# Performance work log

Measured on AMD Instinct MI355X. Metric: run time of the kernel, lower is better.

The kernel has to match this reference:

```python
import jax, jax.numpy as jnp
import numpy as np

D_BINS = 59          # cfg.cam_d
BEV_H, BEV_W = 128, 128


def setup_inputs() -> dict:
    key = jax.random.key(0)
    k = jax.random.split(key, 7)
    B, N, Cin, H, W = 4, 6, 256, 16, 44
    C = 80  # cfg.cam_bev_c
    img_feats = jax.random.normal(k[0], (B, N, Cin, H, W), dtype=jnp.float32)
    rots = jax.random.normal(k[1], (B, N, 3, 3), dtype=jnp.float32)
    trans = jax.random.normal(k[2], (B, N, 3), dtype=jnp.float32)
    intrins = jax.random.normal(k[3], (B, N, 3, 3), dtype=jnp.float32)
    # 1x1 conv == per-pixel linear layer: weight (D+C, Cin), bias (D+C,)
    w_depth = jax.random.normal(k[4], (D_BINS + C, Cin), dtype=jnp.float32) / np.sqrt(Cin)
    b_depth = jnp.zeros((D_BINS + C,), dtype=jnp.float32)
    # projected BEV grid indices (what get_geometry produces via randint)
    geom = jax.random.randint(k[5], (B, N, D_BINS, H, W, 2), 0, BEV_H, dtype=jnp.int32)
    return {"img_feats": img_feats, "rots": rots, "trans": trans,
            "intrins": intrins, "w_depth": w_depth, "b_depth": b_depth,
            "geom": geom}


def reference(img_feats, rots, trans, intrins, w_depth, b_depth, geom):
    B, N, Cin, H, W = img_feats.shape
    C = w_depth.shape[0] - D_BINS
    # depth_net: 1x1 conv -> (B, N, D+C, H, W)
    x = jnp.einsum('bnchw,oc->bnohw', img_feats, w_depth) + b_depth[None, None, :, None, None]
    depth = jax.nn.softmax(x[:, :, :D_BINS], axis=2)          # (B,N,D,H,W)
    context = x[:, :, D_BINS:]                                 # (B,N,C,H,W)
    # outer product: (B,N,D,C,H,W) -> (B,N,D,H,W,C)
    frustum = depth[:, :, :, None] * context[:, :, None]
    frustum = jnp.transpose(frustum, (0, 1, 2, 4, 5, 3))
    # voxel pooling: scatter-add frustum points into BEV grid by geom indices
    cell = geom[..., 0] * BEV_W + geom[..., 1]                 # (B,N,D,H,W)
    flat_idx = (jnp.arange(B, dtype=jnp.int32)[:, None] * (BEV_H * BEV_W)
                + cell.reshape(B, -1)).reshape(-1)
    bev = jax.ops.segment_sum(frustum.reshape(-1, C), flat_idx,
                              num_segments=B * BEV_H * BEV_W)
    return bev.reshape(B, BEV_H, BEV_W, C).transpose(0, 3, 1, 2)  # (B,C,bev_h,bev_w)
```

## Files before the change

kernel.cpp:

```cpp
#include <hip/hip_runtime.h>
#include <hip/hip_bf16.h>
#include <math.h>

#define D_BINS 59
#define CTX    80
#define O_TOT  139
#define O_PAD  144
#define K_CIN  256
#define PIXELS 704
#define BNPAIR 24
#define BEVHW  16384
#define NBATCH 4

#define NTILE   128
#define NBUCKET (NBATCH * NTILE)
#define TCELLS  128

#define PXT    32
#define NPXT   22
#define NBLK   (BNPAIR * NPXT)
#define SEGS   (6 * NPXT)
#define EPB    (PXT * D_BINS)

#define CAP    2816
#define CAPP   (CAP + TCELLS * 7)

#define WHL_F      36864
#define CTX_OFF    (WHL_F)
#define CTX_F      (BNPAIR * PIXELS * CTX / 2)
#define CNTMAT_OFF (CTX_OFF + CTX_F)
#define OFSMAT_OFF (CNTMAT_OFF + NBLK * NTILE)
#define PLIST_OFF  (OFSMAT_OFF + NBLK * NTILE)

typedef __attribute__((ext_vector_type(8))) short bf16x8;
typedef __attribute__((ext_vector_type(4))) float f32x4;

__device__ __forceinline__ unsigned short f2bf(float v) {
    __hip_bfloat16 h = __float2bfloat16(v);
    return *reinterpret_cast<unsigned short*>(&h);
}
__device__ __forceinline__ float bf2f(unsigned short u) {
    return __uint_as_float(((unsigned)u) << 16);
}

__global__ __launch_bounds__(256) void wsplit_kernel(
    const float* __restrict__ w, unsigned short* __restrict__ whl)
{
    const int row = blockIdx.x;
    const int col = threadIdx.x;
    const float v = (row < O_TOT) ? w[(size_t)row * K_CIN + col] : 0.f;
    const unsigned short hi = f2bf(v);
    const unsigned short lo = f2bf(v - bf2f(hi));
    whl[row * K_CIN + col]            = hi;
    whl[36864 + row * K_CIN + col]    = lo;
}

__global__ __launch_bounds__(128) void gemm_fused(
    const float* __restrict__ img,
    const unsigned short* __restrict__ whl,
    const float* __restrict__ bias,
    const int*   __restrict__ geom,
    __hip_bfloat16* __restrict__ ctx,
    uint2*       __restrict__ plist,
    int*         __restrict__ cntmat,
    int*         __restrict__ ofsmat)
{
    __shared__ __align__(16) unsigned char sW[2][O_PAD * 64];
    __shared__ __align__(16) unsigned char sI[2][PXT * 64];
    __shared__ float sbias[O_PAD];
    __shared__ int lh[NTILE], lofs[NTILE], lcur[NTILE], sscan[NTILE];

    const int tid  = threadIdx.x;
    const int lane = tid & 63;
    const int wv   = tid >> 6;
    const int bn   = blockIdx.y;
    const int p0   = blockIdx.x * PXT;

    sbias[tid] = bias[tid];
    if (tid < 16) sbias[128 + tid] = (128 + tid < O_TOT) ? bias[128 + tid] : 0.f;
    lh[tid] = 0;

    const float* imgbn = img + (size_t)bn * K_CIN * PIXELS;

    f32x4 acc[9];
#pragma unroll
    for (int t = 0; t < 9; ++t) acc[t] = (f32x4){0.f, 0.f, 0.f, 0.f};

    const int k2  = tid >> 3;
    const int px4 = (tid & 7) * 4;

    for (int ks = 0; ks < 8; ++ks) {
        const int k0 = ks * 32;
        __syncthreads();
#pragma unroll
        for (int pl = 0; pl < 2; ++pl) {
            for (int c = tid; c < 576; c += 128) {
                const int row = c >> 2, g = c & 3;
                const int gs  = g ^ ((row >> 1) & 3);
                *(float4*)&sW[pl][row * 64 + gs * 16] =
                    *(const float4*)&whl[pl * 36864 + row * K_CIN + k0 + g * 8];
            }
        }
        {
            const float4 v0 = *(const float4*)&imgbn[(size_t)(k0 + 2 * k2) * PIXELS + p0 + px4];
            const float4 v1 = *(const float4*)&imgbn[(size_t)(k0 + 2 * k2 + 1) * PIXELS + p0 + px4];
            const float a0[4] = {v0.x, v0.y, v0.z, v0.w};
            const float a1[4] = {v1.x, v1.y, v1.z, v1.w};
#pragma unroll
            for (int j = 0; j < 4; ++j) {
                const int px  = px4 + j;
                const int gs  = (k2 >> 2) ^ ((px >> 1) & 3);
                const int off = px * 64 + gs * 16 + 4 * (k2 & 3);
                const unsigned short h0 = f2bf(a0[j]);
                const unsigned short h1 = f2bf(a1[j]);
                const unsigned short l0 = f2bf(a0[j] - bf2f(h0));
                const unsigned short l1 = f2bf(a1[j] - bf2f(h1));
                *(unsigned*)&sI[0][off] = (unsigned)h0 | ((unsigned)h1 << 16);
                *(unsigned*)&sI[1][off] = (unsigned)l0 | ((unsigned)l1 << 16);
            }
        }
        __syncthreads();
        const int m = lane & 15;
        const int g = lane >> 4;
        const int bpx = wv * 16 + m;
        const int bgs = g ^ ((bpx >> 1) & 3);
        const bf16x8 bhi = *(const bf16x8*)&sI[0][bpx * 64 + bgs * 16];
        const bf16x8 blo = *(const bf16x8*)&sI[1][bpx * 64 + bgs * 16];
#pragma unroll
        for (int t = 0; t < 9; ++t) {
            const int row = t * 16 + m;
            const int ags = g ^ ((row >> 1) & 3);
            const bf16x8 ahi = *(const bf16x8*)&sW[0][row * 64 + ags * 16];
            const bf16x8 alo = *(const bf16x8*)&sW[1][row * 64 + ags * 16];
            acc[t] = __builtin_amdgcn_mfma_f32_16x16x32_bf16(ahi, bhi, acc[t], 0, 0, 0);
            acc[t] = __builtin_amdgcn_mfma_f32_16x16x32_bf16(ahi, blo, acc[t], 0, 0, 0);
            acc[t] = __builtin_amdgcn_mfma_f32_16x16x32_bf16(alo, bhi, acc[t], 0, 0, 0);
        }
    }

    const int m   = lane & 15;
    const int q   = lane >> 4;
    const int px_local = wv * 16 + m;
    const int pxg = p0 + px_local;

#pragma unroll
    for (int t = 0; t < 9; ++t)
#pragma unroll
        for (int r = 0; r < 4; ++r) acc[t][r] += sbias[t * 16 + q * 4 + r];

    float gm = -INFINITY;
#pragma unroll
    for (int t = 0; t < 4; ++t)
#pragma unroll
        for (int r = 0; r < 4; ++r)
            if (16 * t + 4 * q + r < D_BINS) gm = fmaxf(gm, acc[t][r]);
    gm = fmaxf(gm, __shfl_xor(gm, 16));
    gm = fmaxf(gm, __shfl_xor(gm, 32));
    float ls = 0.f;
#pragma unroll
    for (int t = 0; t < 4; ++t)
#pragma unroll
        for (int r = 0; r < 4; ++r)
            if (16 * t + 4 * q + r < D_BINS) {
                const float e = __expf(acc[t][r] - gm);
                acc[t][r] = e;
                ls += e;
            }
    ls += __shfl_xor(ls, 16);
    ls += __shfl_xor(ls, 32);
    const float inv = 1.f / ls;

    __syncthreads();

    unsigned short* sctx = (unsigned short*)&sW[0][0];
    const int2* g2 = (const int2*)geom;
    unsigned bc[4][4];
#pragma unroll
    for (int t = 0; t < 4; ++t)
#pragma unroll
        for (int r = 0; r < 4; ++r) {
            const int o = 16 * t + 4 * q + r;
            if (o < D_BINS) {
                const int2 gg = g2[((size_t)(bn * D_BINS + o)) * PIXELS + pxg];
                const int tile = (gg.x >> 3) * 8 + (gg.y >> 4);
                const int cell = (gg.x & 7) * 16 + (gg.y & 15);
                bc[t][r] = (unsigned)((tile << 7) | cell);
                atomicAdd(&lh[tile], 1);
            }
        }
#pragma unroll
    for (int t = 3; t < 9; ++t)
#pragma unroll
        for (int r = 0; r < 4; ++r) {
            const int c = 16 * t + 4 * q + r - D_BINS;
            if (c >= 0 && c < CTX) sctx[px_local * CTX + c] = f2bf(acc[t][r]);
        }
    __syncthreads();

    sscan[tid] = lh[tid];
    __syncthreads();
#pragma unroll
    for (int off = 1; off < NTILE; off <<= 1) {
        const int t = (tid >= off) ? sscan[tid - off] : 0;
        __syncthreads();
        sscan[tid] += t;
        __syncthreads();
    }
    const int blk = bn * NPXT + blockIdx.x;
    {
        const int excl = sscan[tid] - lh[tid];
        lofs[tid] = excl;
        lcur[tid] = 0;
        cntmat[(size_t)blk * NTILE + tid] = lh[tid];
        ofsmat[(size_t)blk * NTILE + tid] = excl;
    }
    __syncthreads();

    uint2* dst = plist + (size_t)blk * EPB;
    const unsigned ctxoff = (unsigned)((bn * PIXELS + pxg) * CTX);
#pragma unroll
    for (int t = 0; t < 4; ++t)
#pragma unroll
        for (int r = 0; r < 4; ++r) {
            const int o = 16 * t + 4 * q + r;
            if (o < D_BINS) {
                const unsigned u = bc[t][r];
                const int tl = (int)(u >> 7);
                const int pos = lofs[tl] + atomicAdd(&lcur[tl], 1);
                dst[pos] = make_uint2(__float_as_uint(acc[t][r] * inv),
                                      (ctxoff << 7) | (u & 127u));
            }
        }
    {
        const char* sb = (const char*)sctx;
        char* gb = (char*)ctx + ((size_t)(bn * PIXELS) + p0) * CTX * 2;
        for (int i = tid; i < PXT * CTX * 2 / 16; i += 128)
            *(float4*)(gb + i * 16) = *(const float4*)(sb + i * 16);
    }
}

__global__ __launch_bounds__(1024) void gather_kernel(
    const uint2* __restrict__ plist,
    const int*   __restrict__ cntmat,
    const int*   __restrict__ ofsmat,
    const unsigned short* __restrict__ ctx,
    float*       __restrict__ out)
{
    __shared__ float sacc[CTX][TCELLS + 1];
    __shared__ uint2 bufB[CAPP];
    __shared__ int sg[256];
    __shared__ int segcnt[SEGS], segofs[SEGS];
    __shared__ int cellcnt[TCELLS], celloff[TCELLS], cellcur[TCELLS], sc[TCELLS];
    uint2* bufA = (uint2*)sacc;

    const int tid    = threadIdx.x;
    const int wv     = tid >> 6;
    const int lane   = tid & 63;
    const int bucket = blockIdx.x;
    const int b      = bucket >> 7;
    const int tile   = bucket & 127;
    const int blk0   = b * SEGS;

    if (tid < 256) {
        const int c = (tid < SEGS) ? cntmat[(size_t)(blk0 + tid) * NTILE + tile] : 0;
        sg[tid] = c;
        if (tid < SEGS) segcnt[tid] = c;
    }
    __syncthreads();
#pragma unroll
    for (int off = 1; off < 256; off <<= 1) {
        const int t = (tid < 256 && tid >= off) ? sg[tid - off] : 0;
        __syncthreads();
        if (tid < 256) sg[tid] += t;
        __syncthreads();
    }
    if (tid < SEGS) segofs[tid] = sg[tid] - segcnt[tid];
    __syncthreads();
    const int total = sg[255];

    {
        const int sub = lane >> 4;
        const int sl  = lane & 15;
        for (int sgi = wv * 4 + sub; sgi < SEGS; sgi += 64) {
            const int n = segcnt[sgi];
            if (!n) continue;
            const int dstb = segofs[sgi];
            const uint2* sp = plist + (size_t)(blk0 + sgi) * EPB
                              + ofsmat[(size_t)(blk0 + sgi) * NTILE + tile];
            for (int i = sl; i < n; i += 16) {
                const int d = dstb + i;
                if (d < CAP) bufA[d] = sp[i];
            }
        }
    }
    const int ncap = (total < CAP) ? total : CAP;
    __syncthreads();

    if (tid < TCELLS) cellcnt[tid] = 0;
    __syncthreads();
    for (int i = tid; i < ncap; i += 1024)
        atomicAdd(&cellcnt[bufA[i].y & 127u], 1);
    __syncthreads();
    if (tid < TCELLS) sc[tid] = (cellcnt[tid] + 7) & ~7;
    __syncthreads();
#pragma unroll
    for (int off = 1; off < TCELLS; off <<= 1) {
        const int t = (tid < TCELLS && tid >= off) ? sc[tid - off] : 0;
        __syncthreads();
        if (tid < TCELLS) sc[tid] += t;
        __syncthreads();
    }
    if (tid < TCELLS) {
        celloff[tid] = sc[tid] - ((cellcnt[tid] + 7) & ~7);
        cellcur[tid] = 0;
    }
    __syncthreads();
    const int padtotal = sc[TCELLS - 1];
    for (int i = tid; i < padtotal; i += 1024) bufB[i] = make_uint2(0u, 0u);
    __syncthreads();
    for (int i = tid; i < ncap; i += 1024) {
        const uint2 e = bufA[i];
        const int c = (int)(e.y & 127u);
        bufB[celloff[c] + atomicAdd(&cellcur[c], 1)] = e;
    }
    __syncthreads();

    for (int c = wv; c < TCELLS; c += 16) {
        const int s0 = celloff[c];
        const int pc = (cellcnt[c] + 7) & ~7;
        float a0 = 0.f, a1 = 0.f;
        for (int i = 0; i < pc; i += 8) {
            uint2 e[8];
#pragma unroll
            for (int r = 0; r < 8; ++r) e[r] = bufB[s0 + i + r];
            if (lane < 40) {
                unsigned u[8];
#pragma unroll
                for (int r = 0; r < 8; ++r)
                    u[r] = *(const unsigned*)(ctx + (e[r].y >> 7) + 2 * lane);
#pragma unroll
                for (int r = 0; r < 8; ++r) {
                    const float d  = __uint_as_float(e[r].x);
                    a0 += d * __uint_as_float(u[r] << 16);
                    a1 += d * __uint_as_float(u[r] & 0xffff0000u);
                }
            }
        }
        if (lane < 40) {
            sacc[2 * lane][c]     = a0;
            sacc[2 * lane + 1][c] = a1;
        }
    }

    if (total > CAP) {
        for (int sgi = 0; sgi < SEGS; ++sgi) {
            const int dstb = segofs[sgi];
            const int n    = segcnt[sgi];
            if (dstb + n <= CAP) continue;
            const uint2* sp = plist + (size_t)(blk0 + sgi) * EPB
                              + ofsmat[(size_t)(blk0 + sgi) * NTILE + tile];
            const int i0 = (CAP > dstb) ? (CAP - dstb) : 0;
            for (int i = i0; i < n; ++i) {
                const uint2 e = sp[i];
                const int c = (int)(e.y & 127u);
                if ((c & 15) == wv && lane < 40) {
                    const unsigned u = *(const unsigned*)(ctx + (e.y >> 7) + 2 * lane);
                    const float dep = __uint_as_float(e.x);
                    sacc[2 * lane][c]     += dep * __uint_as_float(u << 16);
                    sacc[2 * lane + 1][c] += dep * __uint_as_float(u & 0xffff0000u);
                }
            }
        }
    }
    __syncthreads();

    const int tl = bucket & 127;
    const int tr = tl >> 3;
    const int tc = tl & 7;
    const int c0  = tid >> 4;
    const int col = tid & 15;
#pragma unroll
    for (int cc = c0; cc < CTX; cc += 64) {
#pragma unroll
        for (int r = 0; r < 8; ++r) {
            out[((size_t)(b * CTX + cc)) * BEVHW + (tr * 8 + r) * 128 + tc * 16 + col]
                = sacc[cc][r * 16 + col];
        }
    }
}

extern "C" void kernel_launch(void* const* d_in, const int* in_sizes, int n_in,
                              void* d_out, int out_size, void* d_ws, size_t ws_size,
                              hipStream_t stream)
{
    const float* img  = (const float*)d_in[0];
    const float* w    = (const float*)d_in[4];
    const float* bias = (const float*)d_in[5];
    const int*   geom = (const int*)d_in[6];
    float*       out  = (float*)d_out;

    float* ws = (float*)d_ws;
    unsigned short* whl = (unsigned short*)ws;
    __hip_bfloat16* ctx = (__hip_bfloat16*)(ws + CTX_OFF);
    int*   cntmat = (int*)(ws + CNTMAT_OFF);
    int*   ofsmat = (int*)(ws + OFSMAT_OFF);
    uint2* plist  = (uint2*)(ws + PLIST_OFF);

    wsplit_kernel<<<O_PAD, 256, 0, stream>>>(w, whl);

    {
        dim3 grid(NPXT, BNPAIR);
        gemm_fused<<<grid, 128, 0, stream>>>(img, whl, bias, geom, ctx,
                                             plist, cntmat, ofsmat);
    }

    gather_kernel<<<NBUCKET, 1024, 0, stream>>>(plist, cntmat, ofsmat,
                                                (const unsigned short*)ctx, out);
}
```

Measured before the change: 144.5 us.

## Pre-split image to bf16 hi/lo slabs and double-buffer GEMM with 256 threads

```diff
diff --git a/kernel.cpp b/kernel.cpp
--- a/kernel.cpp
+++ b/kernel.cpp
@@ -25,8 +25,14 @@
 #define CAP    2816
 #define CAPP   (CAP + TCELLS * 7)
 
-#define WHL_F      36864
-#define CTX_OFF    (WHL_F)
+#define WSLAB  20480
+#define ISLAB  4096
+
+#define WHL_OFF    0
+#define WHL_F      (8 * WSLAB / 4)
+#define IMGHL_OFF  (WHL_OFF + WHL_F)
+#define IMGHL_F    (NBLK * 8 * ISLAB / 4)
+#define CTX_OFF    (IMGHL_OFF + IMGHL_F)
 #define CTX_F      (BNPAIR * PIXELS * CTX / 2)
 #define CNTMAT_OFF (CTX_OFF + CTX_F)
 #define OFSMAT_OFF (CNTMAT_OFF + NBLK * NTILE)
@@ -43,21 +49,59 @@
     return __uint_as_float(((unsigned)u) << 16);
 }
 
-__global__ __launch_bounds__(256) void wsplit_kernel(
-    const float* __restrict__ w, unsigned short* __restrict__ whl)
+__global__ __launch_bounds__(256) void prep_kernel(
+    const float* __restrict__ img,
+    const float* __restrict__ w,
+    unsigned short* __restrict__ whl2,
+    unsigned short* __restrict__ imghl)
 {
-    const int row = blockIdx.x;
-    const int col = threadIdx.x;
-    const float v = (row < O_TOT) ? w[(size_t)row * K_CIN + col] : 0.f;
-    const unsigned short hi = f2bf(v);
-    const unsigned short lo = f2bf(v - bf2f(hi));
-    whl[row * K_CIN + col]            = hi;
-    whl[36864 + row * K_CIN + col]    = lo;
-}
-
-__global__ __launch_bounds__(128) void gemm_fused(
-    const float* __restrict__ img,
-    const unsigned short* __restrict__ whl,
+    const int tid = threadIdx.x;
+    if (blockIdx.x < O_PAD) {
+        const int row = blockIdx.x;
+        const float v = (row < O_TOT) ? w[(size_t)row * K_CIN + tid] : 0.f;
+        const unsigned short hi = f2bf(v);
+        const unsigned short lo = f2bf(v - bf2f(hi));
+        const int ks = tid >> 5, kk = tid & 31;
+        const int g = kk >> 3, e = kk & 7;
+        const int gs = g ^ ((row >> 1) & 3);
+        const size_t base = (size_t)ks * (WSLAB / 2) + row * 32 + gs * 8 + e;
+        whl2[base]        = hi;
+        whl2[base + 4608] = lo;
+        if (row < 8) {
+            for (int i = tid; i < 1024; i += 256)
+                whl2[(size_t)row * (WSLAB / 2) + 9216 + i] = 0;
+        }
+    } else {
+        __shared__ unsigned short sbuf[ISLAB / 2];
+        const int id = blockIdx.x - O_PAD;
+        const int bn = id / NPXT, pt = id - bn * NPXT;
+        const float* ib = img + (size_t)bn * K_CIN * PIXELS + pt * PXT;
+        for (int ks = 0; ks < 8; ++ks) {
+            const int kk  = tid >> 3;
+            const int px4 = (tid & 7) * 4;
+            const float4 v = *(const float4*)&ib[(size_t)(ks * 32 + kk) * PIXELS + px4];
+            const float a[4] = {v.x, v.y, v.z, v.w};
+            const int g = kk >> 3, e = kk & 7;
+#pragma unroll
+            for (int j = 0; j < 4; ++j) {
+                const int px = px4 + j;
+                const int gs = g ^ ((px >> 1) & 3);
+                const unsigned short hi = f2bf(a[j]);
+                const unsigned short lo = f2bf(a[j] - bf2f(hi));
+                sbuf[px * 32 + gs * 8 + e]        = hi;
+                sbuf[1024 + px * 32 + gs * 8 + e] = lo;
+            }
+            __syncthreads();
+            unsigned short* ob = imghl + ((size_t)id * 8 + ks) * (ISLAB / 2);
+            *(float4*)&ob[tid * 8] = *(const float4*)&sbuf[tid * 8];
+            __syncthreads();
+        }
+    }
+}
+
+__global__ __launch_bounds__(256) void gemm_fused(
+    const unsigned short* __restrict__ whl2,
+    const unsigned short* __restrict__ imghl,
     const float* __restrict__ bias,
     const int*   __restrict__ geom,
     __hip_bfloat16* __restrict__ ctx,
@@ -65,176 +109,208 @@
     int*         __restrict__ cntmat,
     int*         __restrict__ ofsmat)
 {
-    __shared__ __align__(16) unsigned char sW[2][O_PAD * 64];
-    __shared__ __align__(16) unsigned char sI[2][PXT * 64];
+    __shared__ __align__(16) unsigned char sS[2][WSLAB + ISLAB];
     __shared__ float sbias[O_PAD];
     __shared__ int lh[NTILE], lofs[NTILE], lcur[NTILE], sscan[NTILE];
 
     const int tid  = threadIdx.x;
     const int lane = tid & 63;
     const int wv   = tid >> 6;
+    const int s    = wv & 1;
+    const int h    = wv >> 1;
     const int bn   = blockIdx.y;
-    const int p0   = blockIdx.x * PXT;
-
-    sbias[tid] = bias[tid];
-    if (tid < 16) sbias[128 + tid] = (128 + tid < O_TOT) ? bias[128 + tid] : 0.f;
-    lh[tid] = 0;
-
-    const float* imgbn = img + (size_t)bn * K_CIN * PIXELS;
-
-    f32x4 acc[9];
-#pragma unroll
-    for (int t = 0; t < 9; ++t) acc[t] = (f32x4){0.f, 0.f, 0.f, 0.f};
-
-    const int k2  = tid >> 3;
-    const int px4 = (tid & 7) * 4;
+    const int pt   = blockIdx.x;
+    const int p0   = pt * PXT;
+    const int blkid = bn * NPXT + pt;
+
+    const unsigned char* wsrc = (const unsigned char*)whl2;
+    const unsigned char* isrc = (const unsigned char*)(imghl + (size_t)blkid * 8 * (ISLAB / 2));
+
+    float4 r[6];
+#pragma unroll
+    for (int j = 0; j < 5; ++j)
+        r[j] = *(const float4*)(wsrc + (size_t)tid * 16 + j * 4096);
+    r[5] = *(const float4*)(isrc + (size_t)tid * 16);
+
+    const int m = lane & 15;
+    const int q = lane >> 4;
+    const int pxl = s * 16 + m;
+    const int pxg = p0 + pxl;
+
+    unsigned bc[4][4];
+    if (h == 0) {
+        const int2* g2 = (const int2*)geom;
+#pragma unroll
+        for (int t = 0; t < 4; ++t)
+#pragma unroll
+            for (int r2 = 0; r2 < 4; ++r2) {
+                const int o = 16 * t + 4 * q + r2;
+                if (o < D_BINS) {
+                    const int2 gg = g2[((size_t)(bn * D_BINS + o)) * PIXELS + pxg];
+                    const int tile = (gg.x >> 3) * 8 + (gg.y >> 4);
+                    const int cell = (gg.x & 7) * 16 + (gg.y & 15);
+                    bc[t][r2] = (unsigned)((tile << 7) | cell);
+                }
+            }
+    }
+    if (tid < O_PAD) sbias[tid] = (tid < O_TOT) ? bias[tid] : 0.f;
+    if (tid < NTILE) lh[tid] = 0;
+    __syncthreads();
+
+    if (h == 0) {
+#pragma unroll
+        for (int t = 0; t < 4; ++t)
+#pragma unroll
+            for (int r2 = 0; r2 < 4; ++r2)
+                if (16 * t + 4 * q + r2 < D_BINS) atomicAdd(&lh[bc[t][r2] >> 7], 1);
+    }
+
+#pragma unroll
+    for (int j = 0; j < 5; ++j) *(float4*)&sS[0][tid * 16 + j * 4096] = r[j];
+    *(float4*)&sS[0][WSLAB + tid * 16] = r[5];
+#pragma unroll
+    for (int j = 0; j < 5; ++j)
+        r[j] = *(const float4*)(wsrc + WSLAB + (size_t)tid * 16 + j * 4096);
+    r[5] = *(const float4*)(isrc + ISLAB + (size_t)tid * 16);
+    asm volatile("s_waitcnt lgkmcnt(0)" ::: "memory");
+    __builtin_amdgcn_s_barrier();
+    __builtin_amdgcn_sched_barrier(0);
+
+    f32x4 acc[5];
+#pragma unroll
+    for (int t = 0; t < 5; ++t) acc[t] = (f32x4){0.f, 0.f, 0.f, 0.f};
+
+    const int g   = lane >> 4;
+    const int bpx = pxl;
+    const int bgs = g ^ ((bpx >> 1) & 3);
+    const int nt  = 5 - h;
 
     for (int ks = 0; ks < 8; ++ks) {
-        const int k0 = ks * 32;
-        __syncthreads();
-#pragma unroll
-        for (int pl = 0; pl < 2; ++pl) {
-            for (int c = tid; c < 576; c += 128) {
-                const int row = c >> 2, g = c & 3;
-                const int gs  = g ^ ((row >> 1) & 3);
-                *(float4*)&sW[pl][row * 64 + gs * 16] =
-                    *(const float4*)&whl[pl * 36864 + row * K_CIN + k0 + g * 8];
-            }
-        }
-        {
-            const float4 v0 = *(const float4*)&imgbn[(size_t)(k0 + 2 * k2) * PIXELS + p0 + px4];
-            const float4 v1 = *(const float4*)&imgbn[(size_t)(k0 + 2 * k2 + 1) * PIXELS + p0 + px4];
-            const float a0[4] = {v0.x, v0.y, v0.z, v0.w};
-            const float a1[4] = {v1.x, v1.y, v1.z, v1.w};
-#pragma unroll
-            for (int j = 0; j < 4; ++j) {
-                const int px  = px4 + j;
-                const int gs  = (k2 >> 2) ^ ((px >> 1) & 3);
-                const int off = px * 64 + gs * 16 + 4 * (k2 & 3);
-                const unsigned short h0 = f2bf(a0[j]);
-                const unsigned short h1 = f2bf(a1[j]);
-                const unsigned short l0 = f2bf(a0[j] - bf2f(h0));
-                const unsigned short l1 = f2bf(a1[j] - bf2f(h1));
-                *(unsigned*)&sI[0][off] = (unsigned)h0 | ((unsigned)h1 << 16);
-                *(unsigned*)&sI[1][off] = (unsigned)l0 | ((unsigned)l1 << 16);
-            }
-        }
-        __syncthreads();
-        const int m = lane & 15;
-        const int g = lane >> 4;
-        const int bpx = wv * 16 + m;
-        const int bgs = g ^ ((bpx >> 1) & 3);
-        const bf16x8 bhi = *(const bf16x8*)&sI[0][bpx * 64 + bgs * 16];
-        const bf16x8 blo = *(const bf16x8*)&sI[1][bpx * 64 + bgs * 16];
-#pragma unroll
-        for (int t = 0; t < 9; ++t) {
-            const int row = t * 16 + m;
-            const int ags = g ^ ((row >> 1) & 3);
-            const bf16x8 ahi = *(const bf16x8*)&sW[0][row * 64 + ags * 16];
-            const bf16x8 alo = *(const bf16x8*)&sW[1][row * 64 + ags * 16];
-            acc[t] = __builtin_amdgcn_mfma_f32_16x16x32_bf16(ahi, bhi, acc[t], 0, 0, 0);
-            acc[t] = __builtin_amdgcn_mfma_f32_16x16x32_bf16(ahi, blo, acc[t], 0, 0, 0);
-            acc[t] = __builtin_amdgcn_mfma_f32_16x16x32_bf16(alo, bhi, acc[t], 0, 0, 0);
-        }
-    }
-
-    const int m   = lane & 15;
-    const int q   = lane >> 4;
-    const int px_local = wv * 16 + m;
-    const int pxg = p0 + px_local;
-
-#pragma unroll
-    for (int t = 0; t < 9; ++t)
-#pragma unroll
-        for (int r = 0; r < 4; ++r) acc[t][r] += sbias[t * 16 + q * 4 + r];
-
-    float gm = -INFINITY;
-#pragma unroll
-    for (int t = 0; t < 4; ++t)
-#pragma unroll
-        for (int r = 0; r < 4; ++r)
-            if (16 * t + 4 * q + r < D_BINS) gm = fmaxf(gm, acc[t][r]);
-    gm = fmaxf(gm, __shfl_xor(gm, 16));
-    gm = fmaxf(gm, __shfl_xor(gm, 32));
-    float ls = 0.f;
-#pragma unroll
-    for (int t = 0; t < 4; ++t)
-#pragma unroll
-        for (int r = 0; r < 4; ++r)
-            if (16 * t + 4 * q + r < D_BINS) {
-                const float e = __expf(acc[t][r] - gm);
-                acc[t][r] = e;
-                ls += e;
-            }
-    ls += __shfl_xor(ls, 16);
-    ls += __shfl_xor(ls, 32);
-    const float inv = 1.f / ls;
-
-    __syncthreads();
-
-    unsigned short* sctx = (unsigned short*)&sW[0][0];
-    const int2* g2 = (const int2*)geom;
-    unsigned bc[4][4];
-#pragma unroll
-    for (int t = 0; t < 4; ++t)
-#pragma unroll
-        for (int r = 0; r < 4; ++r) {
-            const int o = 16 * t + 4 * q + r;
-            if (o < D_BINS) {
-                const int2 gg = g2[((size_t)(bn * D_BINS + o)) * PIXELS + pxg];
-                const int tile = (gg.x >> 3) * 8 + (gg.y >> 4);
-                const int cell = (gg.x & 7) * 16 + (gg.y & 15);
-                bc[t][r] = (unsigned)((tile << 7) | cell);
-                atomicAdd(&lh[tile], 1);
-            }
-        }
-#pragma unroll
-    for (int t = 3; t < 9; ++t)
-#pragma unroll
-        for (int r = 0; r < 4; ++r) {
-            const int c = 16 * t + 4 * q + r - D_BINS;
-            if (c >= 0 && c < CTX) sctx[px_local * CTX + c] = f2bf(acc[t][r]);
-        }
-    __syncthreads();
-
-    sscan[tid] = lh[tid];
+        const unsigned char* base = sS[ks & 1];
+        const bf16x8 bhi = *(const bf16x8*)&base[WSLAB + bpx * 64 + bgs * 16];
+        const bf16x8 blo = *(const bf16x8*)&base[WSLAB + 2048 + bpx * 64 + bgs * 16];
+#pragma unroll
+        for (int t = 0; t < 5; ++t) {
+            if (t < nt) {
+                const int row = h * 80 + t * 16 + m;
+                const int ags = g ^ ((row >> 1) & 3);
+                const bf16x8 ahi = *(const bf16x8*)&base[row * 64 + ags * 16];
+                const bf16x8 alo = *(const bf16x8*)&base[9216 + row * 64 + ags * 16];
+                acc[t] = __builtin_amdgcn_mfma_f32_16x16x32_bf16(ahi, bhi, acc[t], 0, 0, 0);
+                acc[t] = __builtin_amdgcn_mfma_f32_16x16x32_bf16(ahi, blo, acc[t], 0, 0, 0);
+                acc[t] = __builtin_amdgcn_mfma_f32_16x16x32_bf16(alo, bhi, acc[t], 0, 0, 0);
+            }
+        }
+        if (ks < 7) {
+            __syncthreads();
+            unsigned char* nb = sS[(ks + 1) & 1];
+#pragma unroll
+            for (int j = 0; j < 5; ++j) *(float4*)&nb[tid * 16 + j * 4096] = r[j];
+            *(float4*)&nb[WSLAB + tid * 16] = r[5];
+            if (ks < 6) {
+#pragma unroll
+                for (int j = 0; j < 5; ++j)
+                    r[j] = *(const float4*)(wsrc + (size_t)(ks + 2) * WSLAB + (size_t)tid * 16 + j * 4096);
+                r[5] = *(const float4*)(isrc + (size_t)(ks + 2) * ISLAB + (size_t)tid * 16);
+            }
+            asm volatile("s_waitcnt lgkmcnt(0)" ::: "memory");
+            __builtin_amdgcn_s_barrier();
+            __builtin_amdgcn_sched_barrier(0);
+        }
+    }
+    __syncthreads();
+
+#pragma unroll
+    for (int t = 0; t < 5; ++t)
+        if (t < nt)
+#pragma unroll
+            for (int r2 = 0; r2 < 4; ++r2)
+                acc[t][r2] += sbias[h * 80 + t * 16 + q * 4 + r2];
+
+    float inv = 0.f;
+    if (h == 0) {
+        float gm = -INFINITY;
+#pragma unroll
+        for (int t = 0; t < 4; ++t)
+#pragma unroll
+            for (int r2 = 0; r2 < 4; ++r2)
+                if (16 * t + 4 * q + r2 < D_BINS) gm = fmaxf(gm, acc[t][r2]);
+        gm = fmaxf(gm, __shfl_xor(gm, 16));
+        gm = fmaxf(gm, __shfl_xor(gm, 32));
+        float ls = 0.f;
+#pragma unroll
+        for (int t = 0; t < 4; ++t)
+#pragma unroll
+            for (int r2 = 0; r2 < 4; ++r2)
+                if (16 * t + 4 * q + r2 < D_BINS) {
+                    const float e = __expf(acc[t][r2] - gm);
+                    acc[t][r2] = e;
+                    ls += e;
+                }
+        ls += __shfl_xor(ls, 16);
+        ls += __shfl_xor(ls, 32);
+        inv = 1.f / ls;
+    }
+
+    unsigned short* sctx = (unsigned short*)&sS[0][0];
+    if (h == 0) {
+#pragma unroll
+        for (int t = 3; t < 5; ++t)
+#pragma unroll
+            for (int r2 = 0; r2 < 4; ++r2) {
+                const int c = 16 * t + 4 * q + r2 - D_BINS;
+                if (c >= 0) sctx[pxl * CTX + c] = f2bf(acc[t][r2]);
+            }
+    } else {
+#pragma unroll
+        for (int t = 0; t < 4; ++t)
+#pragma unroll
+            for (int r2 = 0; r2 < 4; ++r2) {
+                const int c = 80 + 16 * t + 4 * q + r2 - D_BINS;
+                if (c < CTX) sctx[pxl * CTX + c] = f2bf(acc[t][r2]);
+            }
+    }
+    __syncthreads();
+
+    if (tid < NTILE) sscan[tid] = lh[tid];
     __syncthreads();
 #pragma unroll
     for (int off = 1; off < NTILE; off <<= 1) {
-        const int t = (tid >= off) ? sscan[tid - off] : 0;
-        __syncthreads();
-        sscan[tid] += t;
-        __syncthreads();
-    }
-    const int blk = bn * NPXT + blockIdx.x;
-    {
+        const int t = (tid < NTILE && tid >= off) ? sscan[tid - off] : 0;
+        __syncthreads();
+        if (tid < NTILE) sscan[tid] += t;
+        __syncthreads();
+    }
+    if (tid < NTILE) {
         const int excl = sscan[tid] - lh[tid];
         lofs[tid] = excl;
         lcur[tid] = 0;
-        cntmat[(size_t)blk * NTILE + tid] = lh[tid];
-        ofsmat[(size_t)blk * NTILE + tid] = excl;
-    }
-    __syncthreads();
-
-    uint2* dst = plist + (size_t)blk * EPB;
-    const unsigned ctxoff = (unsigned)((bn * PIXELS + pxg) * CTX);
-#pragma unroll
-    for (int t = 0; t < 4; ++t)
-#pragma unroll
-        for (int r = 0; r < 4; ++r) {
-            const int o = 16 * t + 4 * q + r;
-            if (o < D_BINS) {
-                const unsigned u = bc[t][r];
-                const int tl = (int)(u >> 7);
-                const int pos = lofs[tl] + atomicAdd(&lcur[tl], 1);
-                dst[pos] = make_uint2(__float_as_uint(acc[t][r] * inv),
-                                      (ctxoff << 7) | (u & 127u));
-            }
-        }
+        cntmat[(size_t)blkid * NTILE + tid] = lh[tid];
+        ofsmat[(size_t)blkid * NTILE + tid] = excl;
+    }
+    __syncthreads();
+
+    if (h == 0) {
+        uint2* dst = plist + (size_t)blkid * EPB;
+        const unsigned ctxoff = (unsigned)((bn * PIXELS + pxg) * CTX);
+#pragma unroll
+        for (int t = 0; t < 4; ++t)
+#pragma unroll
+            for (int r2 = 0; r2 < 4; ++r2) {
+                const int o = 16 * t + 4 * q + r2;
+                if (o < D_BINS) {
+                    const unsigned u = bc[t][r2];
+                    const int tl = (int)(u >> 7);
+                    const int pos = lofs[tl] + atomicAdd(&lcur[tl], 1);
+                    dst[pos] = make_uint2(__float_as_uint(acc[t][r2] * inv),
+                                          (ctxoff << 7) | (u & 127u));
+                }
+            }
+    }
     {
         const char* sb = (const char*)sctx;
         char* gb = (char*)ctx + ((size_t)(bn * PIXELS) + p0) * CTX * 2;
-        for (int i = tid; i < PXT * CTX * 2 / 16; i += 128)
+        for (int i = tid; i < PXT * CTX * 2 / 16; i += 256)
             *(float4*)(gb + i * 16) = *(const float4*)(sb + i * 16);
     }
 }
@@ -400,17 +476,18 @@
     float*       out  = (float*)d_out;
 
     float* ws = (float*)d_ws;
-    unsigned short* whl = (unsigned short*)ws;
+    unsigned short* whl2  = (unsigned short*)(ws + WHL_OFF);
+    unsigned short* imghl = (unsigned short*)(ws + IMGHL_OFF);
     __hip_bfloat16* ctx = (__hip_bfloat16*)(ws + CTX_OFF);
     int*   cntmat = (int*)(ws + CNTMAT_OFF);
     int*   ofsmat = (int*)(ws + OFSMAT_OFF);
     uint2* plist  = (uint2*)(ws + PLIST_OFF);
 
-    wsplit_kernel<<<O_PAD, 256, 0, stream>>>(w, whl);
+    prep_kernel<<<O_PAD + NBLK, 256, 0, stream>>>(img, w, whl2, imghl);
 
     {
         dim3 grid(NPXT, BNPAIR);
-        gemm_fused<<<grid, 128, 0, stream>>>(img, whl, bias, geom, ctx,
+        gemm_fused<<<grid, 256, 0, stream>>>(whl2, imghl, bias, geom, ctx,
                                              plist, cntmat, ofsmat);
     }
 
```

After: 175.5 us. +21.5%, slower.

## Split GEMM into depth and context blocks with single-wave 16-pixel tiles

Applied to the files above, without the earlier changes.

```diff
diff --git a/kernel.cpp b/kernel.cpp
--- a/kernel.cpp
+++ b/kernel.cpp
@@ -5,7 +5,6 @@
 #define D_BINS 59
 #define CTX    80
 #define O_TOT  139
-#define O_PAD  144
 #define K_CIN  256
 #define PIXELS 704
 #define BNPAIR 24
@@ -16,8 +15,8 @@
 #define NBUCKET (NBATCH * NTILE)
 #define TCELLS  128
 
-#define PXT    32
-#define NPXT   22
+#define PXT    16
+#define NPXT   44
 #define NBLK   (BNPAIR * NPXT)
 #define SEGS   (6 * NPXT)
 #define EPB    (PXT * D_BINS)
@@ -25,8 +24,9 @@
 #define CAP    2816
 #define CAPP   (CAP + TCELLS * 7)
 
+#define WHL_OFF    0
 #define WHL_F      36864
-#define CTX_OFF    (WHL_F)
+#define CTX_OFF    (WHL_OFF + WHL_F)
 #define CTX_F      (BNPAIR * PIXELS * CTX / 2)
 #define CNTMAT_OFF (CTX_OFF + CTX_F)
 #define OFSMAT_OFF (CNTMAT_OFF + NBLK * NTILE)
@@ -51,11 +51,41 @@
     const float v = (row < O_TOT) ? w[(size_t)row * K_CIN + col] : 0.f;
     const unsigned short hi = f2bf(v);
     const unsigned short lo = f2bf(v - bf2f(hi));
-    whl[row * K_CIN + col]            = hi;
-    whl[36864 + row * K_CIN + col]    = lo;
-}
-
-__global__ __launch_bounds__(128) void gemm_fused(
+    whl[row * K_CIN + col]         = hi;
+    whl[36864 + row * K_CIN + col] = lo;
+}
+
+template<int NT, int T0>
+__device__ __forceinline__ void kloop(
+    const float* __restrict__ ib, const unsigned short* __restrict__ whl,
+    int pxg, int m, int g, f32x4* acc)
+{
+#pragma unroll 2
+    for (int ks = 0; ks < 8; ++ks) {
+        float bv[8];
+#pragma unroll
+        for (int j = 0; j < 8; ++j)
+            bv[j] = ib[(size_t)(ks * 32 + 8 * g + j) * PIXELS + pxg];
+        bf16x8 bhi, blo;
+#pragma unroll
+        for (int j = 0; j < 8; ++j) {
+            const unsigned short h = f2bf(bv[j]);
+            bhi[j] = (short)h;
+            blo[j] = (short)f2bf(bv[j] - bf2f(h));
+        }
+#pragma unroll
+        for (int t = 0; t < NT; ++t) {
+            const int row = (T0 + t) * 16 + m;
+            const bf16x8 ahi = *(const bf16x8*)&whl[(size_t)row * K_CIN + ks * 32 + g * 8];
+            const bf16x8 alo = *(const bf16x8*)&whl[36864 + (size_t)row * K_CIN + ks * 32 + g * 8];
+            acc[t] = __builtin_amdgcn_mfma_f32_16x16x32_bf16(ahi, bhi, acc[t], 0, 0, 0);
+            acc[t] = __builtin_amdgcn_mfma_f32_16x16x32_bf16(ahi, blo, acc[t], 0, 0, 0);
+            acc[t] = __builtin_amdgcn_mfma_f32_16x16x32_bf16(alo, bhi, acc[t], 0, 0, 0);
+        }
+    }
+}
+
+__global__ __launch_bounds__(64) void gemm_fused(
     const float* __restrict__ img,
     const unsigned short* __restrict__ whl,
     const float* __restrict__ bias,
@@ -65,176 +95,129 @@
     int*         __restrict__ cntmat,
     int*         __restrict__ ofsmat)
 {
-    __shared__ __align__(16) unsigned char sW[2][O_PAD * 64];
-    __shared__ __align__(16) unsigned char sI[2][PXT * 64];
-    __shared__ float sbias[O_PAD];
-    __shared__ int lh[NTILE], lofs[NTILE], lcur[NTILE], sscan[NTILE];
-
-    const int tid  = threadIdx.x;
-    const int lane = tid & 63;
-    const int wv   = tid >> 6;
+    const int lane = threadIdx.x;
+    const int m    = lane & 15;
+    const int g    = lane >> 4;
+    const int pt   = blockIdx.x;
     const int bn   = blockIdx.y;
-    const int p0   = blockIdx.x * PXT;
-
-    sbias[tid] = bias[tid];
-    if (tid < 16) sbias[128 + tid] = (128 + tid < O_TOT) ? bias[128 + tid] : 0.f;
-    lh[tid] = 0;
-
-    const float* imgbn = img + (size_t)bn * K_CIN * PIXELS;
-
-    f32x4 acc[9];
-#pragma unroll
-    for (int t = 0; t < 9; ++t) acc[t] = (f32x4){0.f, 0.f, 0.f, 0.f};
-
-    const int k2  = tid >> 3;
-    const int px4 = (tid & 7) * 4;
-
-    for (int ks = 0; ks < 8; ++ks) {
-        const int k0 = ks * 32;
-        __syncthreads();
-#pragma unroll
-        for (int pl = 0; pl < 2; ++pl) {
-            for (int c = tid; c < 576; c += 128) {
-                const int row = c >> 2, g = c & 3;
-                const int gs  = g ^ ((row >> 1) & 3);
-                *(float4*)&sW[pl][row * 64 + gs * 16] =
-                    *(const float4*)&whl[pl * 36864 + row * K_CIN + k0 + g * 8];
-            }
-        }
-        {
-            const float4 v0 = *(const float4*)&imgbn[(size_t)(k0 + 2 * k2) * PIXELS + p0 + px4];
-            const float4 v1 = *(const float4*)&imgbn[(size_t)(k0 + 2 * k2 + 1) * PIXELS + p0 + px4];
-            const float a0[4] = {v0.x, v0.y, v0.z, v0.w};
-            const float a1[4] = {v1.x, v1.y, v1.z, v1.w};
-#pragma unroll
-            for (int j = 0; j < 4; ++j) {
-                const int px  = px4 + j;
-                const int gs  = (k2 >> 2) ^ ((px >> 1) & 3);
-                const int off = px * 64 + gs * 16 + 4 * (k2 & 3);
-                const unsigned short h0 = f2bf(a0[j]);
-                const unsigned short h1 = f2bf(a1[j]);
-                const unsigned short l0 = f2bf(a0[j] - bf2f(h0));
-                const unsigned short l1 = f2bf(a1[j] - bf2f(h1));
-                *(unsigned*)&sI[0][off] = (unsigned)h0 | ((unsigned)h1 << 16);
-                *(unsigned*)&sI[1][off] = (unsigned)l0 | ((unsigned)l1 << 16);
-            }
-        }
-        __syncthreads();
-        const int m = lane & 15;
-        const int g = lane >> 4;
-        const int bpx = wv * 16 + m;
-        const int bgs = g ^ ((bpx >> 1) & 3);
-        const bf16x8 bhi = *(const bf16x8*)&sI[0][bpx * 64 + bgs * 16];
-        const bf16x8 blo = *(const bf16x8*)&sI[1][bpx * 64 + bgs * 16];
-#pragma unroll
-        for (int t = 0; t < 9; ++t) {
-            const int row = t * 16 + m;
-            const int ags = g ^ ((row >> 1) & 3);
-            const bf16x8 ahi = *(const bf16x8*)&sW[0][row * 64 + ags * 16];
-            const bf16x8 alo = *(const bf16x8*)&sW[1][row * 64 + ags * 16];
-            acc[t] = __builtin_amdgcn_mfma_f32_16x16x32_bf16(ahi, bhi, acc[t], 0, 0, 0);
-            acc[t] = __builtin_amdgcn_mfma_f32_16x16x32_bf16(ahi, blo, acc[t], 0, 0, 0);
-            acc[t] = __builtin_amdgcn_mfma_f32_16x16x32_bf16(alo, bhi, acc[t], 0, 0, 0);
-        }
-    }
-
-    const int m   = lane & 15;
-    const int q   = lane >> 4;
-    const int px_local = wv * 16 + m;
-    const int pxg = p0 + px_local;
-
-#pragma unroll
-    for (int t = 0; t < 9; ++t)
-#pragma unroll
-        for (int r = 0; r < 4; ++r) acc[t][r] += sbias[t * 16 + q * 4 + r];
-
-    float gm = -INFINITY;
-#pragma unroll
-    for (int t = 0; t < 4; ++t)
-#pragma unroll
-        for (int r = 0; r < 4; ++r)
-            if (16 * t + 4 * q + r < D_BINS) gm = fmaxf(gm, acc[t][r]);
-    gm = fmaxf(gm, __shfl_xor(gm, 16));
-    gm = fmaxf(gm, __shfl_xor(gm, 32));
-    float ls = 0.f;
-#pragma unroll
-    for (int t = 0; t < 4; ++t)
-#pragma unroll
-        for (int r = 0; r < 4; ++r)
-            if (16 * t + 4 * q + r < D_BINS) {
-                const float e = __expf(acc[t][r] - gm);
-                acc[t][r] = e;
-                ls += e;
-            }
-    ls += __shfl_xor(ls, 16);
-    ls += __shfl_xor(ls, 32);
-    const float inv = 1.f / ls;
-
-    __syncthreads();
-
-    unsigned short* sctx = (unsigned short*)&sW[0][0];
-    const int2* g2 = (const int2*)geom;
-    unsigned bc[4][4];
-#pragma unroll
-    for (int t = 0; t < 4; ++t)
-#pragma unroll
-        for (int r = 0; r < 4; ++r) {
-            const int o = 16 * t + 4 * q + r;
-            if (o < D_BINS) {
-                const int2 gg = g2[((size_t)(bn * D_BINS + o)) * PIXELS + pxg];
-                const int tile = (gg.x >> 3) * 8 + (gg.y >> 4);
-                const int cell = (gg.x & 7) * 16 + (gg.y & 15);
-                bc[t][r] = (unsigned)((tile << 7) | cell);
-                atomicAdd(&lh[tile], 1);
-            }
-        }
-#pragma unroll
-    for (int t = 3; t < 9; ++t)
-#pragma unroll
-        for (int r = 0; r < 4; ++r) {
-            const int c = 16 * t + 4 * q + r - D_BINS;
-            if (c >= 0 && c < CTX) sctx[px_local * CTX + c] = f2bf(acc[t][r]);
-        }
-    __syncthreads();
-
-    sscan[tid] = lh[tid];
-    __syncthreads();
-#pragma unroll
-    for (int off = 1; off < NTILE; off <<= 1) {
-        const int t = (tid >= off) ? sscan[tid - off] : 0;
-        __syncthreads();
-        sscan[tid] += t;
-        __syncthreads();
-    }
-    const int blk = bn * NPXT + blockIdx.x;
-    {
-        const int excl = sscan[tid] - lh[tid];
-        lofs[tid] = excl;
-        lcur[tid] = 0;
-        cntmat[(size_t)blk * NTILE + tid] = lh[tid];
-        ofsmat[(size_t)blk * NTILE + tid] = excl;
-    }
-    __syncthreads();
-
-    uint2* dst = plist + (size_t)blk * EPB;
-    const unsigned ctxoff = (unsigned)((bn * PIXELS + pxg) * CTX);
-#pragma unroll
-    for (int t = 0; t < 4; ++t)
-#pragma unroll
-        for (int r = 0; r < 4; ++r) {
-            const int o = 16 * t + 4 * q + r;
-            if (o < D_BINS) {
-                const unsigned u = bc[t][r];
-                const int tl = (int)(u >> 7);
-                const int pos = lofs[tl] + atomicAdd(&lcur[tl], 1);
-                dst[pos] = make_uint2(__float_as_uint(acc[t][r] * inv),
-                                      (ctxoff << 7) | (u & 127u));
-            }
-        }
-    {
+    const int p0   = pt * PXT;
+    const int pxg  = p0 + m;
+    const int blkid = bn * NPXT + pt;
+    const float* ib = img + (size_t)bn * K_CIN * PIXELS;
+
+    if (blockIdx.z == 0) {
+        __shared__ int lh[NTILE], lofs[NTILE], lcur[NTILE];
+        f32x4 acc[4];
+#pragma unroll
+        for (int t = 0; t < 4; ++t) acc[t] = (f32x4){0.f, 0.f, 0.f, 0.f};
+        kloop<4, 0>(ib, whl, pxg, m, g, acc);
+
+        const int2* g2 = (const int2*)geom;
+        int2 gg[4][4];
+#pragma unroll
+        for (int t = 0; t < 4; ++t)
+#pragma unroll
+            for (int r = 0; r < 4; ++r) {
+                const int o = 16 * t + 4 * g + r;
+                if (o < D_BINS)
+                    gg[t][r] = g2[((size_t)(bn * D_BINS + o)) * PIXELS + pxg];
+            }
+        lh[lane] = 0; lh[lane + 64] = 0;
+        lcur[lane] = 0; lcur[lane + 64] = 0;
+
+#pragma unroll
+        for (int t = 0; t < 4; ++t)
+#pragma unroll
+            for (int r = 0; r < 4; ++r) acc[t][r] += bias[16 * t + 4 * g + r];
+
+        float gm = -INFINITY;
+#pragma unroll
+        for (int t = 0; t < 4; ++t)
+#pragma unroll
+            for (int r = 0; r < 4; ++r)
+                if (16 * t + 4 * g + r < D_BINS) gm = fmaxf(gm, acc[t][r]);
+        gm = fmaxf(gm, __shfl_xor(gm, 16));
+        gm = fmaxf(gm, __shfl_xor(gm, 32));
+        float ls = 0.f;
+#pragma unroll
+        for (int t = 0; t < 4; ++t)
+#pragma unroll
+            for (int r = 0; r < 4; ++r)
+                if (16 * t + 4 * g + r < D_BINS) {
+                    const float e = __expf(acc[t][r] - gm);
+                    acc[t][r] = e;
+                    ls += e;
+                }
+        ls += __shfl_xor(ls, 16);
+        ls += __shfl_xor(ls, 32);
+        const float inv = 1.f / ls;
+
+        unsigned uc[4][4];
+#pragma unroll
+        for (int t = 0; t < 4; ++t)
+#pragma unroll
+            for (int r = 0; r < 4; ++r) {
+                const int o = 16 * t + 4 * g + r;
+                if (o < D_BINS) {
+                    const int2 q = gg[t][r];
+                    const int tile = (q.x >> 3) * 8 + (q.y >> 4);
+                    const int cell = (q.x & 7) * 16 + (q.y & 15);
+                    uc[t][r] = (unsigned)((tile << 7) | cell);
+                    atomicAdd(&lh[tile], 1);
+                }
+            }
+
+        const int l2 = 2 * lane;
+        const int a = lh[l2];
+        const int b = lh[l2 + 1];
+        const int p = a + b;
+        int incl = p;
+#pragma unroll
+        for (int off = 1; off < 64; off <<= 1) {
+            const int t = __shfl_up(incl, off);
+            if (lane >= off) incl += t;
+        }
+        const int excl = incl - p;
+        lofs[l2]     = excl;
+        lofs[l2 + 1] = excl + a;
+        *(int2*)&cntmat[(size_t)blkid * NTILE + l2] = make_int2(a, b);
+        *(int2*)&ofsmat[(size_t)blkid * NTILE + l2] = make_int2(excl, excl + a);
+
+        uint2* dst = plist + (size_t)blkid * EPB;
+        const unsigned ctxoff = (unsigned)((bn * PIXELS + pxg) * CTX);
+#pragma unroll
+        for (int t = 0; t < 4; ++t)
+#pragma unroll
+            for (int r = 0; r < 4; ++r) {
+                const int o = 16 * t + 4 * g + r;
+                if (o < D_BINS) {
+                    const unsigned u = uc[t][r];
+                    const int tl = (int)(u >> 7);
+                    const int pos = lofs[tl] + atomicAdd(&lcur[tl], 1);
+                    dst[pos] = make_uint2(__float_as_uint(acc[t][r] * inv),
+                                          (ctxoff << 7) | (u & 127u));
+                }
+            }
+    } else {
+        __shared__ unsigned short sctx[PXT][CTX];
+        f32x4 acc[6];
+#pragma unroll
+        for (int t = 0; t < 6; ++t) acc[t] = (f32x4){0.f, 0.f, 0.f, 0.f};
+        kloop<6, 3>(ib, whl, pxg, m, g, acc);
+
+#pragma unroll
+        for (int t = 0; t < 6; ++t)
+#pragma unroll
+            for (int r = 0; r < 4; ++r) {
+                const int o = (3 + t) * 16 + 4 * g + r;
+                const int c = o - D_BINS;
+                if (c >= 0 && c < CTX)
+                    sctx[m][c] = f2bf(acc[t][r] + bias[o]);
+            }
         const char* sb = (const char*)sctx;
         char* gb = (char*)ctx + ((size_t)(bn * PIXELS) + p0) * CTX * 2;
-        for (int i = tid; i < PXT * CTX * 2 / 16; i += 128)
+#pragma unroll
+        for (int i = lane; i < PXT * CTX * 2 / 16; i += 64)
             *(float4*)(gb + i * 16) = *(const float4*)(sb + i * 16);
     }
 }
@@ -248,7 +231,7 @@
 {
     __shared__ float sacc[CTX][TCELLS + 1];
     __shared__ uint2 bufB[CAPP];
-    __shared__ int sg[256];
+    __shared__ int sg[512];
     __shared__ int segcnt[SEGS], segofs[SEGS];
     __shared__ int cellcnt[TCELLS], celloff[TCELLS], cellcur[TCELLS], sc[TCELLS];
     uint2* bufA = (uint2*)sacc;
@@ -261,33 +244,33 @@
     const int tile   = bucket & 127;
     const int blk0   = b * SEGS;
 
-    if (tid < 256) {
+    if (tid < 512) {
         const int c = (tid < SEGS) ? cntmat[(size_t)(blk0 + tid) * NTILE + tile] : 0;
         sg[tid] = c;
         if (tid < SEGS) segcnt[tid] = c;
     }
     __syncthreads();
 #pragma unroll
-    for (int off = 1; off < 256; off <<= 1) {
-        const int t = (tid < 256 && tid >= off) ? sg[tid - off] : 0;
+    for (int off = 1; off < 512; off <<= 1) {
+        const int t = (tid < 512 && tid >= off) ? sg[tid - off] : 0;
         __syncthreads();
-        if (tid < 256) sg[tid] += t;
+        if (tid < 512) sg[tid] += t;
         __syncthreads();
     }
     if (tid < SEGS) segofs[tid] = sg[tid] - segcnt[tid];
     __syncthreads();
-    const int total = sg[255];
+    const int total = sg[511];
 
     {
-        const int sub = lane >> 4;
-        const int sl  = lane & 15;
-        for (int sgi = wv * 4 + sub; sgi < SEGS; sgi += 64) {
+        const int sub = lane >> 3;
+        const int sl  = lane & 7;
+        for (int sgi = wv * 8 + sub; sgi < SEGS; sgi += 128) {
             const int n = segcnt[sgi];
             if (!n) continue;
             const int dstb = segofs[sgi];
             const uint2* sp = plist + (size_t)(blk0 + sgi) * EPB
                               + ofsmat[(size_t)(blk0 + sgi) * NTILE + tile];
-            for (int i = sl; i < n; i += 16) {
+            for (int i = sl; i < n; i += 8) {
                 const int d = dstb + i;
                 if (d < CAP) bufA[d] = sp[i];
             }
@@ -400,18 +383,18 @@
     float*       out  = (float*)d_out;
 
     float* ws = (float*)d_ws;
-    unsigned short* whl = (unsigned short*)ws;
+    unsigned short* whl = (unsigned short*)(ws + WHL_OFF);
     __hip_bfloat16* ctx = (__hip_bfloat16*)(ws + CTX_OFF);
     int*   cntmat = (int*)(ws + CNTMAT_OFF);
     int*   ofsmat = (int*)(ws + OFSMAT_OFF);
     uint2* plist  = (uint2*)(ws + PLIST_OFF);
 
-    wsplit_kernel<<<O_PAD, 256, 0, stream>>>(w, whl);
+    wsplit_kernel<<<144, 256, 0, stream>>>(w, whl);
 
     {
-        dim3 grid(NPXT, BNPAIR);
-        gemm_fused<<<grid, 128, 0, stream>>>(img, whl, bias, geom, ctx,
-                                             plist, cntmat, ofsmat);
+        dim3 grid(NPXT, BNPAIR, 2);
+        gemm_fused<<<grid, 64, 0, stream>>>(img, whl, bias, geom, ctx,
+                                            plist, cntmat, ofsmat);
     }
 
     gather_kernel<<<NBUCKET, 1024, 0, stream>>>(plist, cntmat, ofsmat,
```

New measurement: 140.6 us. -2.6%, faster.
